# Performance work log

Hardware: AMD Instinct MI355X
Metric: run time of the kernel (lower is better)

## Reference

```python
import jax, jax.numpy as jnp
import numpy as np
import math

B, S, HID = 2, 2048, 2048
NH, NKV = 32, 8
HD = HID // NH  # 64
N_REP = NH // NKV  # 4


def setup_inputs() -> dict:
    key = jax.random.key(0)
    ks = jax.random.split(key, 7)
    sc = 0.02
    return {
        "hidden_states": jax.random.normal(ks[0], (B, S, HID), jnp.float32),
        "cos": jax.random.normal(ks[1], (S, HD), jnp.float32),
        "sin": jax.random.normal(ks[2], (S, HD), jnp.float32),
        "wq": jax.random.normal(ks[3], (NH * HD, HID), jnp.float32) * sc,
        "wk": jax.random.normal(ks[4], (NKV * HD, HID), jnp.float32) * sc,
        "wv": jax.random.normal(ks[5], (NKV * HD, HID), jnp.float32) * sc,
        "wo": jax.random.normal(ks[6], (HID, NH * HD), jnp.float32) * sc,
    }


def _rotate_half(x):
    x1, x2 = jnp.split(x, 2, axis=-1)
    return jnp.concatenate([-x2, x1], axis=-1)


def _apply_rotary(q, k, cos, sin):
    # q: [B,S,NH,HD], k: [B,S,NKV,HD]; cos/sin: [S,HD] broadcast over batch, heads
    c = cos[None, :, None, :]
    s = sin[None, :, None, :]
    return q * c + _rotate_half(q) * s, k * c + _rotate_half(k) * s


def reference(hidden_states, cos, sin, wq, wk, wv, wo):
    x = hidden_states  # [B,S,HID]
    q = jnp.einsum('bsh,dh->bsd', x, wq).reshape(B, S, NH, HD)
    k = jnp.einsum('bsh,dh->bsd', x, wk).reshape(B, S, NKV, HD)
    v = jnp.einsum('bsh,dh->bsd', x, wv).reshape(B, S, NKV, HD)
    q, k = _apply_rotary(q, k, cos, sin)
    # repeat_kv: expand kv heads by N_REP -> [B,S,NH,HD]
    k = jnp.repeat(k, N_REP, axis=2)
    v = jnp.repeat(v, N_REP, axis=2)
    # [B,NH,S,HD]
    q = q.transpose(0, 2, 1, 3)
    k = k.transpose(0, 2, 1, 3)
    v = v.transpose(0, 2, 1, 3)
    scores = jnp.einsum('bhqd,bhkd->bhqk', q, k) / math.sqrt(HD)
    probs = jax.nn.softmax(scores.astype(jnp.float32), axis=-1).astype(q.dtype)
    out = jnp.einsum('bhqk,bhkd->bhqd', probs, v)
    out = out.transpose(0, 2, 1, 3).reshape(B, S, NH * HD)
    return jnp.einsum('bsd,hd->bsh', out, wo)
```

## Files before the change

### kernel.cpp

```cpp
#include <hip/hip_runtime.h>
#include <math.h>

#define B 2
#define S 2048
#define HID 2048
#define NH 32
#define NKV 8
#define HD 64
#define NREP 4

typedef __bf16 bf16_t;
typedef bf16_t bf16x8 __attribute__((ext_vector_type(8)));
typedef bf16_t bf16x2 __attribute__((ext_vector_type(2)));
typedef float floatx4 __attribute__((ext_vector_type(4)));

__device__ __forceinline__ void gld_lds16(const void* g, void* l) {
    __builtin_amdgcn_global_load_lds(
        (const __attribute__((address_space(1))) void*)g,
        (__attribute__((address_space(3))) void*)l, 16, 0, 0);
}

__device__ __forceinline__ int pack2(float a, float b) {
    bf16x2 v; v[0] = (bf16_t)a; v[1] = (bf16_t)b;
    return __builtin_bit_cast(int, v);
}

__global__ __launch_bounds__(256) void cast_all(const float* __restrict__ x,
                                                const float* __restrict__ wq,
                                                const float* __restrict__ wk,
                                                const float* __restrict__ wv,
                                                const float* __restrict__ wo,
                                                bf16_t* __restrict__ xb,
                                                bf16_t* __restrict__ wqkvb,
                                                bf16_t* __restrict__ wob) {
    int gid = blockIdx.x * 256 + threadIdx.x;
    const float* src; bf16_t* dst; int idx;
    if (gid < 1048576)      { src = x;  dst = xb;               idx = gid; }
    else if (gid < 1572864) { src = wq; dst = wqkvb;            idx = gid - 1048576; }
    else if (gid < 1703936) { src = wk; dst = wqkvb + 4194304;  idx = gid - 1572864; }
    else if (gid < 1835008) { src = wv; dst = wqkvb + 5242880;  idx = gid - 1703936; }
    else                    { src = wo; dst = wob;              idx = gid - 1835008; }
    size_t i = (size_t)idx * 8;
    float4 f0 = *(const float4*)(src + i);
    float4 f1 = *(const float4*)(src + i + 4);
    bf16x8 v;
    v[0] = (bf16_t)f0.x; v[1] = (bf16_t)f0.y; v[2] = (bf16_t)f0.z; v[3] = (bf16_t)f0.w;
    v[4] = (bf16_t)f1.x; v[5] = (bf16_t)f1.y; v[6] = (bf16_t)f1.z; v[7] = (bf16_t)f1.w;
    *(bf16x8*)(dst + i) = v;
}

#define TM 128
#define TN 128
#define BK 32

enum { MODE_QKV = 0, MODE_OUT = 2 };

template <int MODE>
__global__ __launch_bounds__(256) void gemm_mfma(const bf16_t* __restrict__ A,
                                                 const bf16_t* __restrict__ W,
                                                 void* __restrict__ outQ,
                                                 bf16_t* __restrict__ outK,
                                                 bf16_t* __restrict__ outV,
                                                 const float* __restrict__ cosp,
                                                 const float* __restrict__ sinp,
                                                 int M, int N, int K) {
    __shared__ __align__(16) bf16_t As[TM * BK];
    __shared__ __align__(16) bf16_t Ws[TN * BK];
    const int t    = threadIdx.x;
    const int wave = t >> 6, lane = t & 63;
    const int quad = lane >> 4, l16 = lane & 15;
    const int m0 = blockIdx.y * TM, n0 = blockIdx.x * TN;
    const int wm = (wave >> 1) * 64, wn = (wave & 1) * 64;

    floatx4 zero4 = {0.f, 0.f, 0.f, 0.f};
    floatx4 acc[4][4];
    #pragma unroll
    for (int i = 0; i < 4; ++i)
        #pragma unroll
        for (int j = 0; j < 4; ++j) acc[i][j] = zero4;

    const bf16_t* Arow = A + (size_t)(m0 + (t >> 2)) * K + (t & 3) * 8;
    const bf16_t* Wrow = W + (size_t)(n0 + (t >> 2)) * K + (t & 3) * 8;
    bf16_t* Asl = As + t * 8;
    bf16_t* Wsl = Ws + t * 8;

    for (int k0 = 0; k0 < K; k0 += BK) {
        gld_lds16(Arow + k0,          Asl);
        gld_lds16(Arow + 64 * K + k0, Asl + 64 * BK);
        gld_lds16(Wrow + k0,          Wsl);
        gld_lds16(Wrow + 64 * K + k0, Wsl + 64 * BK);
        __syncthreads();
        bf16x8 af[4], bfr[4];
        #pragma unroll
        for (int i = 0; i < 4; ++i)
            af[i] = *(bf16x8*)&As[(wm + i * 16 + l16) * BK + quad * 8];
        #pragma unroll
        for (int j = 0; j < 4; ++j)
            bfr[j] = *(bf16x8*)&Ws[(wn + j * 16 + l16) * BK + quad * 8];
        #pragma unroll
        for (int i = 0; i < 4; ++i)
            #pragma unroll
            for (int j = 0; j < 4; ++j)
                acc[i][j] = __builtin_amdgcn_mfma_f32_16x16x32_bf16(af[i], bfr[j], acc[i][j], 0, 0, 0);
        __syncthreads();
    }

    if constexpr (MODE == MODE_OUT) {
        float* C = (float*)outQ;
        #pragma unroll
        for (int i = 0; i < 4; ++i)
            #pragma unroll
            for (int r = 0; r < 4; ++r) {
                int row = m0 + wm + i * 16 + quad * 4 + r;
                #pragma unroll
                for (int j = 0; j < 4; ++j)
                    C[(size_t)row * N + n0 + wn + j * 16 + l16] = acc[i][j][r];
            }
    } else {
        const int hh = (n0 + wn) / 64;
        #pragma unroll
        for (int i = 0; i < 4; ++i)
            #pragma unroll
            for (int r = 0; r < 4; ++r) {
                int m = m0 + wm + i * 16 + quad * 4 + r;
                int b = m / S, s = m % S;
                if (hh < NH + NKV) {
                    bf16_t* base;
                    float sc;
                    if (hh < NH) {
                        base = (bf16_t*)outQ + ((size_t)(b * NH + hh) * S + s) * HD;
                        sc = 0.18033688011f;
                    } else {
                        base = outK + ((size_t)(b * NKV + (hh - NH)) * S + s) * HD;
                        sc = 1.0f;
                    }
                    #pragma unroll
                    for (int j = 0; j < 2; ++j) {
                        int d = j * 16 + l16;
                        float x1 = acc[i][j][r], x2 = acc[i][j + 2][r];
                        float c1 = cosp[s * HD + d],      s1 = sinp[s * HD + d];
                        float c2 = cosp[s * HD + d + 32], s2 = sinp[s * HD + d + 32];
                        base[d]      = (bf16_t)((x1 * c1 - x2 * s1) * sc);
                        base[d + 32] = (bf16_t)((x2 * c2 + x1 * s2) * sc);
                    }
                } else {
                    int kvh = hh - NH - NKV;
                    bf16_t* vb = outV + ((size_t)(b * NKV + kvh) * HD) * S + s;
                    #pragma unroll
                    for (int j = 0; j < 4; ++j)
                        vb[(size_t)(j * 16 + l16) * S] = (bf16_t)acc[i][j][r];
                }
            }
    }
}

#define PP 72
__global__ __launch_bounds__(128, 2) void attn_mfma(const bf16_t* __restrict__ Q,
                                                    const bf16_t* __restrict__ Kb,
                                                    const bf16_t* __restrict__ Vt,
                                                    bf16_t* __restrict__ Ob) {
    __shared__ __align__(16) bf16_t Ks[2 * 64 * 32];
    __shared__ __align__(16) bf16_t Vs[2 * 64 * 32];
    __shared__ __align__(16) bf16_t Pq[2 * 64 * PP];
    const int t    = threadIdx.x;
    const int wave = t >> 6, lane = t & 63;
    const int quad = lane >> 4, l16 = lane & 15;
    const int bh = blockIdx.y, b = bh / NH, h = bh % NH, kvh = h / NREP;
    const int q0 = blockIdx.x * 128;

    const bf16_t* qbase = Q + ((size_t)bh * S + q0 + wave * 64) * HD;
    const bf16_t* kbase = Kb + ((size_t)(b * NKV + kvh) * S) * HD;
    const bf16_t* vbase = Vt + (size_t)(b * NKV + kvh) * HD * S;
    bf16_t* Pqw = Pq + wave * 64 * PP;

    bf16x8 qf[4][2];
    #pragma unroll
    for (int qj = 0; qj < 4; ++qj)
        #pragma unroll
        for (int ks = 0; ks < 2; ++ks)
            qf[qj][ks] = *(const bf16x8*)(qbase + (size_t)(qj * 16 + l16) * HD + ks * 32 + quad * 8);

    floatx4 zero4 = {0.f, 0.f, 0.f, 0.f};
    floatx4 of[4][4];
    #pragma unroll
    for (int di = 0; di < 4; ++di)
        #pragma unroll
        for (int qj = 0; qj < 4; ++qj) of[di][qj] = zero4;
    float lsum[4] = {0.f, 0.f, 0.f, 0.f};

    const int r4 = t >> 2;
    const int c8 = (t & 3) * 8;

    for (int kt = 0; kt < S; kt += 64) {
        __syncthreads();
        #pragma unroll
        for (int ks = 0; ks < 2; ++ks) {
            gld_lds16(kbase + (size_t)(kt + r4) * HD + ks * 32 + c8,      Ks + ks * 2048 + t * 8);
            gld_lds16(kbase + (size_t)(kt + 32 + r4) * HD + ks * 32 + c8, Ks + ks * 2048 + 1024 + t * 8);
            gld_lds16(vbase + (size_t)r4 * S + kt + ks * 32 + c8,         Vs + ks * 2048 + t * 8);
            gld_lds16(vbase + (size_t)(32 + r4) * S + kt + ks * 32 + c8,  Vs + ks * 2048 + 1024 + t * 8);
        }
        __syncthreads();

        #pragma unroll
        for (int ki = 0; ki < 4; ++ki) {
            bf16x8 ka0 = *(bf16x8*)&Ks[0 * 2048 + (ki * 16 + l16) * 32 + quad * 8];
            bf16x8 ka1 = *(bf16x8*)&Ks[1 * 2048 + (ki * 16 + l16) * 32 + quad * 8];
            floatx4 sf[4];
            #pragma unroll
            for (int qj = 0; qj < 4; ++qj) sf[qj] = zero4;
            #pragma unroll
            for (int qj = 0; qj < 4; ++qj)
                sf[qj] = __builtin_amdgcn_mfma_f32_16x16x32_bf16(ka0, qf[qj][0], sf[qj], 0, 0, 0);
            #pragma unroll
            for (int qj = 0; qj < 4; ++qj)
                sf[qj] = __builtin_amdgcn_mfma_f32_16x16x32_bf16(ka1, qf[qj][1], sf[qj], 0, 0, 0);
            #pragma unroll
            for (int qj = 0; qj < 4; ++qj) {
                float p0 = __builtin_amdgcn_exp2f(sf[qj][0]);
                float p1 = __builtin_amdgcn_exp2f(sf[qj][1]);
                float p2 = __builtin_amdgcn_exp2f(sf[qj][2]);
                float p3 = __builtin_amdgcn_exp2f(sf[qj][3]);
                lsum[qj] += (p0 + p1) + (p2 + p3);
                int2 pk; pk.x = pack2(p0, p1); pk.y = pack2(p2, p3);
                *(int2*)&Pqw[(qj * 16 + l16) * PP + ki * 16 + quad * 4] = pk;
            }
        }

        #pragma unroll
        for (int ks = 0; ks < 2; ++ks) {
            bf16x8 pb[4], va[4];
            #pragma unroll
            for (int qj = 0; qj < 4; ++qj)
                pb[qj] = *(bf16x8*)&Pqw[(qj * 16 + l16) * PP + ks * 32 + quad * 8];
            #pragma unroll
            for (int di = 0; di < 4; ++di)
                va[di] = *(bf16x8*)&Vs[ks * 2048 + (di * 16 + l16) * 32 + quad * 8];
            #pragma unroll
            for (int di = 0; di < 4; ++di)
                #pragma unroll
                for (int qj = 0; qj < 4; ++qj)
                    of[di][qj] = __builtin_amdgcn_mfma_f32_16x16x32_bf16(va[di], pb[qj], of[di][qj], 0, 0, 0);
        }
    }

    #pragma unroll
    for (int qj = 0; qj < 4; ++qj) {
        float ls = lsum[qj];
        ls += __shfl_xor(ls, 16);
        ls += __shfl_xor(ls, 32);
        float inv = 1.f / ls;
        int q = q0 + wave * 64 + qj * 16 + l16;
        bf16_t* ob = Ob + ((size_t)(b * S + q)) * HID + h * HD;
        #pragma unroll
        for (int di = 0; di < 4; ++di) {
            int2 pk;
            pk.x = pack2(of[di][qj][0] * inv, of[di][qj][1] * inv);
            pk.y = pack2(of[di][qj][2] * inv, of[di][qj][3] * inv);
            *(int2*)(ob + di * 16 + quad * 4) = pk;
        }
    }
}

extern "C" void kernel_launch(void* const* d_in, const int* in_sizes, int n_in,
                              void* d_out, int out_size, void* d_ws, size_t ws_size,
                              hipStream_t stream) {
    const float* x    = (const float*)d_in[0];
    const float* cosp = (const float*)d_in[1];
    const float* sinp = (const float*)d_in[2];
    const float* wq   = (const float*)d_in[3];
    const float* wk   = (const float*)d_in[4];
    const float* wv   = (const float*)d_in[5];
    const float* wo   = (const float*)d_in[6];
    float* out = (float*)d_out;

    char* ws = (char*)d_ws;
    bf16_t* xb    = (bf16_t*)(ws);
    bf16_t* kb    = (bf16_t*)(ws + 16777216);
    bf16_t* vtb   = (bf16_t*)(ws + 20971520);
    bf16_t* wqkvb = (bf16_t*)(ws + 25165824);
    bf16_t* wob   = (bf16_t*)(ws + 37748736);
    bf16_t* attb  = (bf16_t*)(ws);
    bf16_t* qb    = (bf16_t*)d_out;

    const int M = B * S;

    cast_all<<<9216, 256, 0, stream>>>(x, wq, wk, wv, wo, xb, wqkvb, wob);

    gemm_mfma<MODE_QKV><<<dim3(3072 / TN, M / TM), 256, 0, stream>>>(
        xb, wqkvb, (void*)qb, kb, vtb, cosp, sinp, M, 3072, HID);

    attn_mfma<<<dim3(S / 128, B * NH), 128, 0, stream>>>(qb, kb, vtb, attb);

    gemm_mfma<MODE_OUT><<<dim3(2048 / TN, M / TM), 256, 0, stream>>>(
        attb, wob, (void*)out, nullptr, nullptr, nullptr, nullptr, M, 2048, HID);
}
```

Before: 333.5 us.

## Split attention along keys with combine kernel, shrink P buffer, deepen GEMM K-step

Attention now splits the key range into two halves across blockIdx.z. Each half writes unnormalized partial outputs and row sums, and a new combine kernel adds them and normalizes. This doubles the block count for better CU occupancy, and a smaller P scratch buffer plus a 3-block occupancy hint raise residency further. The GEMM now loads BK=64 per iteration in two 32-wide sub-tiles, which halves the barrier count. The costs are an extra kernel launch, extra global traffic for the partial outputs, and bf16 rounding of unnormalized partials. The exp without max subtraction was already present.

```diff
diff --git a/kernel.cpp b/kernel.cpp
--- a/kernel.cpp
+++ b/kernel.cpp
@@ -51,7 +51,7 @@
 
 #define TM 128
 #define TN 128
-#define BK 32
+#define BK 64
 
 enum { MODE_QKV = 0, MODE_OUT = 2 };
 
@@ -64,8 +64,8 @@
                                                  const float* __restrict__ cosp,
                                                  const float* __restrict__ sinp,
                                                  int M, int N, int K) {
-    __shared__ __align__(16) bf16_t As[TM * BK];
-    __shared__ __align__(16) bf16_t Ws[TN * BK];
+    __shared__ __align__(16) bf16_t As[2 * TM * 32];
+    __shared__ __align__(16) bf16_t Ws[2 * TN * 32];
     const int t    = threadIdx.x;
     const int wave = t >> 6, lane = t & 63;
     const int quad = lane >> 4, l16 = lane & 15;
@@ -79,29 +79,35 @@
         #pragma unroll
         for (int j = 0; j < 4; ++j) acc[i][j] = zero4;
 
-    const bf16_t* Arow = A + (size_t)(m0 + (t >> 2)) * K + (t & 3) * 8;
-    const bf16_t* Wrow = W + (size_t)(n0 + (t >> 2)) * K + (t & 3) * 8;
-    bf16_t* Asl = As + t * 8;
-    bf16_t* Wsl = Ws + t * 8;
+    const int r4 = t >> 2;
+    const int c8 = (t & 3) * 8;
+    const bf16_t* Arow = A + (size_t)(m0 + r4) * K + c8;
+    const bf16_t* Wrow = W + (size_t)(n0 + r4) * K + c8;
 
     for (int k0 = 0; k0 < K; k0 += BK) {
-        gld_lds16(Arow + k0,          Asl);
-        gld_lds16(Arow + 64 * K + k0, Asl + 64 * BK);
-        gld_lds16(Wrow + k0,          Wsl);
-        gld_lds16(Wrow + 64 * K + k0, Wsl + 64 * BK);
+        #pragma unroll
+        for (int ks = 0; ks < 2; ++ks) {
+            gld_lds16(Arow + k0 + ks * 32,          As + ks * 4096 + t * 8);
+            gld_lds16(Arow + 64 * K + k0 + ks * 32, As + ks * 4096 + 2048 + t * 8);
+            gld_lds16(Wrow + k0 + ks * 32,          Ws + ks * 4096 + t * 8);
+            gld_lds16(Wrow + 64 * K + k0 + ks * 32, Ws + ks * 4096 + 2048 + t * 8);
+        }
         __syncthreads();
-        bf16x8 af[4], bfr[4];
-        #pragma unroll
-        for (int i = 0; i < 4; ++i)
-            af[i] = *(bf16x8*)&As[(wm + i * 16 + l16) * BK + quad * 8];
-        #pragma unroll
-        for (int j = 0; j < 4; ++j)
-            bfr[j] = *(bf16x8*)&Ws[(wn + j * 16 + l16) * BK + quad * 8];
-        #pragma unroll
-        for (int i = 0; i < 4; ++i)
+        #pragma unroll
+        for (int ks = 0; ks < 2; ++ks) {
+            bf16x8 af[4], bfr[4];
+            #pragma unroll
+            for (int i = 0; i < 4; ++i)
+                af[i] = *(bf16x8*)&As[ks * 4096 + (wm + i * 16 + l16) * 32 + quad * 8];
             #pragma unroll
             for (int j = 0; j < 4; ++j)
-                acc[i][j] = __builtin_amdgcn_mfma_f32_16x16x32_bf16(af[i], bfr[j], acc[i][j], 0, 0, 0);
+                bfr[j] = *(bf16x8*)&Ws[ks * 4096 + (wn + j * 16 + l16) * 32 + quad * 8];
+            #pragma unroll
+            for (int i = 0; i < 4; ++i)
+                #pragma unroll
+                for (int j = 0; j < 4; ++j)
+                    acc[i][j] = __builtin_amdgcn_mfma_f32_16x16x32_bf16(af[i], bfr[j], acc[i][j], 0, 0, 0);
+        }
         __syncthreads();
     }
 
@@ -154,11 +160,13 @@
     }
 }
 
-#define PP 72
-__global__ __launch_bounds__(128, 2) void attn_mfma(const bf16_t* __restrict__ Q,
+#define PP 40
+__global__ __launch_bounds__(128, 3) void attn_mfma(const bf16_t* __restrict__ Q,
                                                     const bf16_t* __restrict__ Kb,
                                                     const bf16_t* __restrict__ Vt,
-                                                    bf16_t* __restrict__ Ob) {
+                                                    bf16_t* __restrict__ Ou0,
+                                                    bf16_t* __restrict__ Ou1,
+                                                    float* __restrict__ lsb) {
     __shared__ __align__(16) bf16_t Ks[2 * 64 * 32];
     __shared__ __align__(16) bf16_t Vs[2 * 64 * 32];
     __shared__ __align__(16) bf16_t Pq[2 * 64 * PP];
@@ -167,11 +175,14 @@
     const int quad = lane >> 4, l16 = lane & 15;
     const int bh = blockIdx.y, b = bh / NH, h = bh % NH, kvh = h / NREP;
     const int q0 = blockIdx.x * 128;
+    const int split = blockIdx.z;
+    const int kt0 = split * (S / 2);
 
     const bf16_t* qbase = Q + ((size_t)bh * S + q0 + wave * 64) * HD;
     const bf16_t* kbase = Kb + ((size_t)(b * NKV + kvh) * S) * HD;
     const bf16_t* vbase = Vt + (size_t)(b * NKV + kvh) * HD * S;
     bf16_t* Pqw = Pq + wave * 64 * PP;
+    bf16_t* Ou = split ? Ou1 : Ou0;
 
     bf16x8 qf[4][2];
     #pragma unroll
@@ -191,7 +202,7 @@
     const int r4 = t >> 2;
     const int c8 = (t & 3) * 8;
 
-    for (int kt = 0; kt < S; kt += 64) {
+    for (int kt = kt0; kt < kt0 + S / 2; kt += 64) {
         __syncthreads();
         #pragma unroll
         for (int ks = 0; ks < 2; ++ks) {
@@ -203,39 +214,39 @@
         __syncthreads();
 
         #pragma unroll
-        for (int ki = 0; ki < 4; ++ki) {
-            bf16x8 ka0 = *(bf16x8*)&Ks[0 * 2048 + (ki * 16 + l16) * 32 + quad * 8];
-            bf16x8 ka1 = *(bf16x8*)&Ks[1 * 2048 + (ki * 16 + l16) * 32 + quad * 8];
-            floatx4 sf[4];
-            #pragma unroll
-            for (int qj = 0; qj < 4; ++qj) sf[qj] = zero4;
+        for (int ph = 0; ph < 2; ++ph) {
+            #pragma unroll
+            for (int kio = 0; kio < 2; ++kio) {
+                int ki = ph * 2 + kio;
+                bf16x8 ka0 = *(bf16x8*)&Ks[0 * 2048 + (ki * 16 + l16) * 32 + quad * 8];
+                bf16x8 ka1 = *(bf16x8*)&Ks[1 * 2048 + (ki * 16 + l16) * 32 + quad * 8];
+                floatx4 sf[4];
+                #pragma unroll
+                for (int qj = 0; qj < 4; ++qj) sf[qj] = zero4;
+                #pragma unroll
+                for (int qj = 0; qj < 4; ++qj)
+                    sf[qj] = __builtin_amdgcn_mfma_f32_16x16x32_bf16(ka0, qf[qj][0], sf[qj], 0, 0, 0);
+                #pragma unroll
+                for (int qj = 0; qj < 4; ++qj)
+                    sf[qj] = __builtin_amdgcn_mfma_f32_16x16x32_bf16(ka1, qf[qj][1], sf[qj], 0, 0, 0);
+                #pragma unroll
+                for (int qj = 0; qj < 4; ++qj) {
+                    float p0 = __builtin_amdgcn_exp2f(sf[qj][0]);
+                    float p1 = __builtin_amdgcn_exp2f(sf[qj][1]);
+                    float p2 = __builtin_amdgcn_exp2f(sf[qj][2]);
+                    float p3 = __builtin_amdgcn_exp2f(sf[qj][3]);
+                    lsum[qj] += (p0 + p1) + (p2 + p3);
+                    int2 pk; pk.x = pack2(p0, p1); pk.y = pack2(p2, p3);
+                    *(int2*)&Pqw[(qj * 16 + l16) * PP + kio * 16 + quad * 4] = pk;
+                }
+            }
+            bf16x8 pb[4], va[4];
             #pragma unroll
             for (int qj = 0; qj < 4; ++qj)
-                sf[qj] = __builtin_amdgcn_mfma_f32_16x16x32_bf16(ka0, qf[qj][0], sf[qj], 0, 0, 0);
-            #pragma unroll
-            for (int qj = 0; qj < 4; ++qj)
-                sf[qj] = __builtin_amdgcn_mfma_f32_16x16x32_bf16(ka1, qf[qj][1], sf[qj], 0, 0, 0);
-            #pragma unroll
-            for (int qj = 0; qj < 4; ++qj) {
-                float p0 = __builtin_amdgcn_exp2f(sf[qj][0]);
-                float p1 = __builtin_amdgcn_exp2f(sf[qj][1]);
-                float p2 = __builtin_amdgcn_exp2f(sf[qj][2]);
-                float p3 = __builtin_amdgcn_exp2f(sf[qj][3]);
-                lsum[qj] += (p0 + p1) + (p2 + p3);
-                int2 pk; pk.x = pack2(p0, p1); pk.y = pack2(p2, p3);
-                *(int2*)&Pqw[(qj * 16 + l16) * PP + ki * 16 + quad * 4] = pk;
-            }
-        }
-
-        #pragma unroll
-        for (int ks = 0; ks < 2; ++ks) {
-            bf16x8 pb[4], va[4];
-            #pragma unroll
-            for (int qj = 0; qj < 4; ++qj)
-                pb[qj] = *(bf16x8*)&Pqw[(qj * 16 + l16) * PP + ks * 32 + quad * 8];
+                pb[qj] = *(bf16x8*)&Pqw[(qj * 16 + l16) * PP + quad * 8];
             #pragma unroll
             for (int di = 0; di < 4; ++di)
-                va[di] = *(bf16x8*)&Vs[ks * 2048 + (di * 16 + l16) * 32 + quad * 8];
+                va[di] = *(bf16x8*)&Vs[ph * 2048 + (di * 16 + l16) * 32 + quad * 8];
             #pragma unroll
             for (int di = 0; di < 4; ++di)
                 #pragma unroll
@@ -249,17 +260,36 @@
         float ls = lsum[qj];
         ls += __shfl_xor(ls, 16);
         ls += __shfl_xor(ls, 32);
-        float inv = 1.f / ls;
         int q = q0 + wave * 64 + qj * 16 + l16;
-        bf16_t* ob = Ob + ((size_t)(b * S + q)) * HID + h * HD;
+        if (lane < 16)
+            lsb[split * 131072 + bh * 2048 + q] = ls;
+        bf16_t* ob = Ou + ((size_t)(b * S + q)) * HID + h * HD;
         #pragma unroll
         for (int di = 0; di < 4; ++di) {
             int2 pk;
-            pk.x = pack2(of[di][qj][0] * inv, of[di][qj][1] * inv);
-            pk.y = pack2(of[di][qj][2] * inv, of[di][qj][3] * inv);
+            pk.x = pack2(of[di][qj][0], of[di][qj][1]);
+            pk.y = pack2(of[di][qj][2], of[di][qj][3]);
             *(int2*)(ob + di * 16 + quad * 4) = pk;
         }
     }
+}
+
+__global__ __launch_bounds__(256) void combine_kernel(bf16_t* __restrict__ Ou0,
+                                                      const bf16_t* __restrict__ Ou1,
+                                                      const float* __restrict__ lsb) {
+    size_t i = ((size_t)blockIdx.x * 256 + threadIdx.x) * 8;
+    if (i >= (size_t)B * S * HID) return;
+    int h = (int)((i >> 6) & 31);
+    int q = (int)((i >> 11) & 2047);
+    int b = (int)(i >> 22);
+    int li = (b * 32 + h) * 2048 + q;
+    float inv = 1.f / (lsb[li] + lsb[131072 + li]);
+    bf16x8 a = *(bf16x8*)(Ou0 + i);
+    bf16x8 c = *(const bf16x8*)(Ou1 + i);
+    bf16x8 r;
+    #pragma unroll
+    for (int j = 0; j < 8; ++j) r[j] = (bf16_t)(((float)a[j] + (float)c[j]) * inv);
+    *(bf16x8*)(Ou0 + i) = r;
 }
 
 extern "C" void kernel_launch(void* const* d_in, const int* in_sizes, int n_in,
@@ -280,8 +310,10 @@
     bf16_t* vtb   = (bf16_t*)(ws + 20971520);
     bf16_t* wqkvb = (bf16_t*)(ws + 25165824);
     bf16_t* wob   = (bf16_t*)(ws + 37748736);
+    float*  lsb   = (float*)(ws + 46137344);
     bf16_t* attb  = (bf16_t*)(ws);
     bf16_t* qb    = (bf16_t*)d_out;
+    bf16_t* ou1   = (bf16_t*)((char*)d_out + 16777216);
 
     const int M = B * S;
 
@@ -290,7 +322,9 @@
     gemm_mfma<MODE_QKV><<<dim3(3072 / TN, M / TM), 256, 0, stream>>>(
         xb, wqkvb, (void*)qb, kb, vtb, cosp, sinp, M, 3072, HID);
 
-    attn_mfma<<<dim3(S / 128, B * NH), 128, 0, stream>>>(qb, kb, vtb, attb);
+    attn_mfma<<<dim3(S / 128, B * NH, 2), 128, 0, stream>>>(qb, kb, vtb, attb, ou1, lsb);
+
+    combine_kernel<<<4096, 256, 0, stream>>>(attb, ou1, lsb);
 
     gemm_mfma<MODE_OUT><<<dim3(2048 / TN, M / TM), 256, 0, stream>>>(
         attb, wob, (void*)out, nullptr, nullptr, nullptr, nullptr, M, 2048, HID);
```

Result: slower. 516.4 us (+54.9%).
